# Performance work log

Measured on AMD Instinct MI355X. Metric: run time of the kernel, lower is better.

Reference implementation:

```python
import jax, jax.numpy as jnp
import numpy as np

N = 100_000      # nodes
E = 500_000      # bonds
DN = 128         # dim_node_embedding
DB = 64          # dim_bond_embedding
NTOK = 4         # num_bond_token
DIN = 2 * DN + 2 * DB  # 384
LEAKY = 0.001
LN_EPS = 1e-5
DIST_MAX = 20.0
STEP = 0.5


def _lrelu(v):
    return jnp.where(v >= 0, v, LEAKY * v)


def _layernorm(v, w, b):
    m = v.mean(-1, keepdims=True)
    var = ((v - m) ** 2).mean(-1, keepdims=True)
    return (v - m) / jnp.sqrt(var + LN_EPS) * w + b


def setup_inputs() -> dict:
    key = jax.random.key(0)
    ks = jax.random.split(key, 20)
    x = jax.random.normal(ks[0], (N, 3), dtype=jnp.float32) * 3.0
    pos = jax.random.normal(ks[1], (N, 3), dtype=jnp.float32)
    node_embedding = jax.random.normal(ks[2], (N, DN), dtype=jnp.float32)
    i0 = jax.random.randint(ks[3], (E,), 0, N)
    off = jax.random.randint(ks[4], (E,), 1, N)  # nonzero -> no self-bonds
    bond_index = jnp.stack([i0, (i0 + off) % N], axis=1).astype(jnp.int32)
    bond_types = jax.random.randint(ks[5], (E,), 0, NTOK).astype(jnp.int32)
    s = 0.02
    params = dict(
        bond_emb=jax.random.normal(ks[6], (NTOK, DB), dtype=jnp.float32),
        W0=jax.random.normal(ks[7], (DIN, DN), dtype=jnp.float32) * s,
        b0=jnp.zeros((DN,), jnp.float32),
        W1=jax.random.normal(ks[8], (DN, DN), dtype=jnp.float32) * s,
        b1=jnp.zeros((DN,), jnp.float32),
        ln1_w=jnp.ones((DN,), jnp.float32),
        ln1_b=jnp.zeros((DN,), jnp.float32),
        W2=jax.random.normal(ks[9], (DN, DN), dtype=jnp.float32) * s,
        b2=jnp.zeros((DN,), jnp.float32),
        ln2_w=jnp.ones((DN,), jnp.float32),
        ln2_b=jnp.zeros((DN,), jnp.float32),
        Wo=jax.random.normal(ks[10], (DN, 2), dtype=jnp.float32) * s,
        bo=jnp.zeros((2,), jnp.float32),
    )
    return dict(x=x, pos=pos, node_embedding=node_embedding,
                bond_index=bond_index, bond_types=bond_types, **params)


def reference(x, pos, node_embedding, bond_index, bond_types,
              bond_emb, W0, b0, W1, b1, ln1_w, ln1_b,
              W2, b2, ln2_w, ln2_b, Wo, bo):
    i = bond_index[:, 0]
    j = bond_index[:, 1]

    # ---- BondLength geometry ----
    diff = x[i] - x[j]                                   # [E,3]
    dist = jnp.linalg.norm(diff, axis=-1, keepdims=True)  # [E,1]
    u = diff / dist                                       # [E,3] unit j->i? (i-j)/d
    direction = jnp.stack([u, -u], axis=-1)               # [E,3,2]

    # ---- Smearing (gaussian RBF + overflow bin, normalized) ----
    offset = jnp.linspace(0.0, DIST_MAX, DB - 1, dtype=jnp.float32)  # [63]
    delta = DIST_MAX / (DB - 2)
    coeff = -0.5 / (delta * delta)
    rbf = jnp.exp(coeff * (dist - offset) ** 2)            # [E,63]
    ovf = (dist >= DIST_MAX).astype(x.dtype)               # [E,1]
    smear = jnp.concatenate([rbf, ovf], axis=-1)           # [E,64]
    smear = smear / smear.sum(axis=-1, keepdims=True)

    # ---- Edge MLP (LeakyMLP, num_layer=2, dim_end=2) ----
    feat = jnp.concatenate(
        [node_embedding[i], node_embedding[j], bond_emb[bond_types], smear],
        axis=-1)                                           # [E,384]
    h = _lrelu(feat @ W0 + b0)
    h = _lrelu(_layernorm(h @ W1 + b1, ln1_w, ln1_b))
    h = _lrelu(_layernorm(h @ W2 + b2, ln2_w, ln2_b))
    force = h @ Wo + bo                                    # [E,2]

    # ---- position update (scatter-add) ----
    update = force[:, None, :] * direction                 # [E,3,2]
    pos = pos.at[i].add(STEP * update[..., 0])
    pos = pos.at[j].add(STEP * update[..., 1])
    return pos
```

## Files before the change

### kernel.cpp

```cpp
#include <hip/hip_runtime.h>
#include <stdint.h>

#define N_EDGES 500000
#define N_NODES 100000
#define PREP_NG 2
#define TBINS 1280

typedef __attribute__((ext_vector_type(8))) short short8;
typedef __attribute__((ext_vector_type(4))) float floatx4;

__device__ __forceinline__ uint16_t f2bf(float f) {
  union { float f; uint32_t u; } cv; cv.f = f;
  uint32_t u = cv.u;
  return (uint16_t)((u + 0x7FFFu + ((u >> 16) & 1u)) >> 16);
}
__device__ __forceinline__ uint32_t pk2bf(float lo, float hi) {
  return __builtin_amdgcn_perm(__float_as_uint(hi), __float_as_uint(lo), 0x07060302u);
}
__device__ __forceinline__ uint16_t bftrunc(float f) {
  return (uint16_t)(__float_as_uint(f) >> 16);
}
__device__ __forceinline__ float bf2f_lo(uint32_t u) { return __uint_as_float(u << 16); }
__device__ __forceinline__ float bf2f_hi(uint32_t u) { return __uint_as_float(u & 0xFFFF0000u); }
__device__ __forceinline__ float lrelu(float v) { return fmaxf(v, 0.001f * v); }

__device__ __forceinline__ void gload_lds16(const uint16_t* g, uint16_t* l) {
  __builtin_amdgcn_global_load_lds(
      (const __attribute__((address_space(1))) void*)g,
      (__attribute__((address_space(3))) void*)l, 16, 0, 0);
}

__global__ void prep0_kernel(const float* __restrict__ W0, const float* __restrict__ b0,
                             const float* __restrict__ W1, const float* __restrict__ W2,
                             const float* __restrict__ bemb,
                             uint16_t* __restrict__ w0ab, uint16_t* __restrict__ w1f,
                             uint16_t* __restrict__ w2f, float* __restrict__ be0f,
                             const float* __restrict__ pos, float* __restrict__ out, int npos) {
  int id = blockIdx.x * 256 + threadIdx.x;
  if (id < 32768) {
    int f = id;
    int j = f & 7, lane = (f >> 3) & 63, ntt = (f >> 9) & 15, ks = f >> 13;
    int k = ks * 32 + (lane >> 4) * 8 + j;
    int row = (ntt < 8) ? k : (128 + k);
    int col = (ntt & 7) * 16 + (lane & 15);
    w0ab[f] = f2bf(W0[row * 128 + col]);
  } else if (id < 49152) {
    int f = id - 32768;
    int j = f & 7, lane = (f >> 3) & 63, nt = (f >> 9) & 7, ks = f >> 12;
    int k = ks * 32 + (lane >> 4) * 8 + j;
    w1f[f] = f2bf(W1[k * 128 + nt * 16 + (lane & 15)]);
  } else if (id < 65536) {
    int f = id - 49152;
    int j = f & 7, lane = (f >> 3) & 63, nt = (f >> 9) & 7, ks = f >> 12;
    int k = ks * 32 + (lane >> 4) * 8 + j;
    w2f[f] = f2bf(W2[k * 128 + nt * 16 + (lane & 15)]);
  } else if (id < 66048) {
    int t = id - 65536; int ty = t >> 7, n = t & 127;
    float s = b0[n];
    for (int kk = 0; kk < 64; ++kk) s += bemb[ty * 64 + kk] * W0[(256 + kk) * 128 + n];
    be0f[t] = s;
  } else if (id - 66048 < npos) {
    out[id - 66048] = pos[id - 66048];
  }
}

__global__ void prep_t_kernel(const float* __restrict__ W0, const float* __restrict__ be0f,
                              uint16_t* __restrict__ T) {
  __shared__ float rbf[64];
  int b = blockIdx.x;
  int t = threadIdx.x;
  float dist = (float)b * (1.0f / 32.0f);
  const float delta = 20.0f / 62.0f;
  const float coeff = -0.5f / (delta * delta);
  if (t < 64) {
    float v;
    if (t < 63) { float d = dist - (float)t * delta; v = __expf(coeff * d * d); }
    else v = (dist >= 20.0f) ? 1.0f : 0.0f;
    rbf[t] = v;
  }
  __syncthreads();
  float sum = 0.0f;
  for (int k = 0; k < 64; ++k) sum += rbf[k];
  float rs = 1.0f / sum;
  for (int o = t; o < 512; o += 256) {
    int ty = o >> 7, n = o & 127;
    float s = be0f[ty * 128 + n];
    for (int k = 0; k < 64; ++k) s += rbf[k] * rs * W0[(320 + k) * 128 + n];
    T[((size_t)(ty * TBINS + b)) * 128 + n] = f2bf(s);
  }
}

__global__ __attribute__((amdgpu_flat_work_group_size(256, 256), amdgpu_waves_per_eu(1, 4)))
void prep_p_kernel(const float* __restrict__ nemb, const uint16_t* __restrict__ w0ab,
                   uint16_t* __restrict__ Pa, uint16_t* __restrict__ Pb) {
  __shared__ __align__(16) uint16_t aLds[4 * PREP_NG * 16 * 136];
  const int tid = threadIdx.x;
  const int lane = tid & 63;
  const int wave = tid >> 6;
  const int n15 = lane & 15;
  const int quad = lane >> 4;
  uint16_t* myA = aLds + wave * (PREP_NG * 16 * 136);
  const int base = blockIdx.x * (64 * PREP_NG) + wave * (16 * PREP_NG);

  {
    const int le = lane >> 2, sub = lane & 3;
#pragma unroll
    for (int it = 0; it < PREP_NG; ++it) {
      int r = base + it * 16 + le; if (r >= N_NODES) r = N_NODES - 1;
      const float4* src = (const float4*)(nemb + (size_t)r * 128);
#pragma unroll
      for (int g = 0; g < 4; ++g) {
        float4 a = src[sub * 8 + g * 2], b = src[sub * 8 + g * 2 + 1];
        uint4 pk;
        pk.x = pk2bf(a.x, a.y); pk.y = pk2bf(a.z, a.w);
        pk.z = pk2bf(b.x, b.y); pk.w = pk2bf(b.z, b.w);
        *(uint4*)(myA + (it * 16 + le) * 136 + sub * 32 + g * 8) = pk;
      }
    }
  }

  const short8* wfv = (const short8*)w0ab + lane;
#pragma unroll
  for (int q = 0; q < 4; ++q) {
    short8 bfr[16];
#pragma unroll
    for (int ks = 0; ks < 4; ++ks)
#pragma unroll
      for (int nq = 0; nq < 4; ++nq)
        bfr[ks * 4 + nq] = wfv[(ks * 16 + q * 4 + nq) * 64];
#pragma unroll
    for (int it = 0; it < PREP_NG; ++it) {
      floatx4 acc[4];
#pragma unroll
      for (int nq = 0; nq < 4; ++nq) acc[nq] = (floatx4){0.f, 0.f, 0.f, 0.f};
#pragma unroll
      for (int ks = 0; ks < 4; ++ks) {
        short8 a = *(const short8*)(myA + (it * 16 + n15) * 136 + ks * 32 + quad * 8);
#pragma unroll
        for (int nq = 0; nq < 4; ++nq)
          acc[nq] = __builtin_amdgcn_mfma_f32_16x16x32_bf16(a, bfr[ks * 4 + nq], acc[nq], 0, 0, 0);
      }
      uint16_t* dst = (q < 2) ? Pa : Pb;
      int cbase = ((q & 1) * 4) * 16 + n15;
#pragma unroll
      for (int nq = 0; nq < 4; ++nq) {
        int c = cbase + nq * 16;
#pragma unroll
        for (int r = 0; r < 4; ++r) {
          int row = base + it * 16 + quad * 4 + r;
          if (row < N_NODES) dst[(size_t)row * 128 + c] = bftrunc(acc[nq][r]);
        }
      }
    }
  }
}

__device__ __forceinline__ void gemm_lds(const uint16_t* ws, const uint16_t* aRow,
                                         int lane, floatx4* acc) {
  short8 a[4];
#pragma unroll
  for (int ks = 0; ks < 4; ++ks) a[ks] = *(const short8*)(aRow + ks * 32);
#pragma unroll
  for (int ks = 0; ks < 4; ++ks)
#pragma unroll
    for (int nt = 0; nt < 8; ++nt) {
      short8 b = *(const short8*)(ws + (ks * 8 + nt) * 512 + lane * 8);
      acc[nt] = __builtin_amdgcn_mfma_f32_16x16x32_bf16(a[ks], b, acc[nt], 0, 0, 0);
    }
}

__global__ __attribute__((amdgpu_flat_work_group_size(256, 256)))
void bond_mlp_kernel(const float* __restrict__ x,
                     const int* __restrict__ bidx, const int* __restrict__ btyp,
                     const uint16_t* __restrict__ Pa, const uint16_t* __restrict__ Pb,
                     const uint16_t* __restrict__ Tt, const uint16_t* __restrict__ w1f,
                     const uint16_t* __restrict__ w2f,
                     const float* __restrict__ b1, const float* __restrict__ ln1w,
                     const float* __restrict__ ln1b,
                     const float* __restrict__ b2, const float* __restrict__ ln2w,
                     const float* __restrict__ ln2b,
                     const float* __restrict__ Wo, const float* __restrict__ bo,
                     float* __restrict__ out) {
  __shared__ __align__(16) uint16_t wstage[16384];
  __shared__ __align__(16) uint16_t hA_all[4 * 16 * 136];
  __shared__ float u_lds[64][3];
  __shared__ int ij_lds[64][2];

  const int tid = threadIdx.x;
  const int lane = tid & 63;
  const int wave = tid >> 6;
  const int n15 = lane & 15;
  const int quad = lane >> 4;

  uint16_t* hA = hA_all + wave * (16 * 136);

#pragma unroll
  for (int j = 0; j < 8; ++j)
    gload_lds16(w1f + (wave * 8 + j) * 512 + lane * 8, wstage + (wave * 8 + j) * 512);

  {
    const int le = lane >> 2, sub = lane & 3;
    const int gr = wave * 16 + le;
    const int ge = blockIdx.x * 64 + gr;
    const bool valid = ge < N_EDGES;
    int vi = 0, vj = 0, bt = 0;
    if (valid) { vi = bidx[2 * ge]; vj = bidx[2 * ge + 1]; bt = btyp[ge]; }
    float dx, dy, dz;
    if (valid) {
      dx = x[3 * vi]     - x[3 * vj];
      dy = x[3 * vi + 1] - x[3 * vj + 1];
      dz = x[3 * vi + 2] - x[3 * vj + 2];
    } else { dx = 1.0f; dy = 0.0f; dz = 0.0f; }
    float dist = sqrtf(dx * dx + dy * dy + dz * dz);
    float rinv = 1.0f / dist;
    if (sub == 0) {
      u_lds[gr][0] = dx * rinv; u_lds[gr][1] = dy * rinv; u_lds[gr][2] = dz * rinv;
      ij_lds[gr][0] = vi; ij_lds[gr][1] = vj;
    }
    float fb = fminf(dist, 39.5f) * 32.0f;
    int bi = (int)fb;
    float w = fb - (float)bi;
    const uint4* pa = (const uint4*)(Pa + (size_t)vi * 128 + sub * 32);
    const uint4* pb = (const uint4*)(Pb + (size_t)vj * 128 + sub * 32);
    const uint16_t* trow = Tt + ((size_t)(bt * TBINS + bi)) * 128 + sub * 32;
    const uint4* t0p = (const uint4*)trow;
    const uint4* t1p = (const uint4*)(trow + 128);
#pragma unroll
    for (int g = 0; g < 4; ++g) {
      uint4 av = pa[g], bv = pb[g], t0 = t0p[g], t1 = t1p[g];
      uint4 pk;
      {
        float lo = bf2f_lo(av.x) + bf2f_lo(bv.x), hi = bf2f_hi(av.x) + bf2f_hi(bv.x);
        float l0 = bf2f_lo(t0.x), l1 = bf2f_lo(t1.x), h0 = bf2f_hi(t0.x), h1 = bf2f_hi(t1.x);
        pk.x = pk2bf(lrelu(lo + l0 + w * (l1 - l0)), lrelu(hi + h0 + w * (h1 - h0)));
      }
      {
        float lo = bf2f_lo(av.y) + bf2f_lo(bv.y), hi = bf2f_hi(av.y) + bf2f_hi(bv.y);
        float l0 = bf2f_lo(t0.y), l1 = bf2f_lo(t1.y), h0 = bf2f_hi(t0.y), h1 = bf2f_hi(t1.y);
        pk.y = pk2bf(lrelu(lo + l0 + w * (l1 - l0)), lrelu(hi + h0 + w * (h1 - h0)));
      }
      {
        float lo = bf2f_lo(av.z) + bf2f_lo(bv.z), hi = bf2f_hi(av.z) + bf2f_hi(bv.z);
        float l0 = bf2f_lo(t0.z), l1 = bf2f_lo(t1.z), h0 = bf2f_hi(t0.z), h1 = bf2f_hi(t1.z);
        pk.z = pk2bf(lrelu(lo + l0 + w * (l1 - l0)), lrelu(hi + h0 + w * (h1 - h0)));
      }
      {
        float lo = bf2f_lo(av.w) + bf2f_lo(bv.w), hi = bf2f_hi(av.w) + bf2f_hi(bv.w);
        float l0 = bf2f_lo(t0.w), l1 = bf2f_lo(t1.w), h0 = bf2f_hi(t0.w), h1 = bf2f_hi(t1.w);
        pk.w = pk2bf(lrelu(lo + l0 + w * (l1 - l0)), lrelu(hi + h0 + w * (h1 - h0)));
      }
      *(uint4*)(hA + le * 136 + sub * 32 + g * 8) = pk;
    }
  }
  __syncthreads();

  const uint16_t* aRow = hA + n15 * 136 + quad * 8;

  floatx4 acc[8];
#pragma unroll
  for (int nt = 0; nt < 8; ++nt) acc[nt] = (floatx4){0.f, 0.f, 0.f, 0.f};
  gemm_lds(wstage, aRow, lane, acc);

  __syncthreads();
#pragma unroll
  for (int j = 0; j < 8; ++j)
    gload_lds16(w2f + (wave * 8 + j) * 512 + lane * 8, wstage + (wave * 8 + j) * 512);

  {
    float bv[8], wv[8], bb2[8];
#pragma unroll
    for (int nt = 0; nt < 8; ++nt) {
      int col = nt * 16 + n15;
      bv[nt] = b1[col]; wv[nt] = ln1w[col]; bb2[nt] = ln1b[col];
    }
    float s[4] = {0,0,0,0}, q[4] = {0,0,0,0};
#pragma unroll
    for (int nt = 0; nt < 8; ++nt)
#pragma unroll
      for (int r = 0; r < 4; ++r) { float v = acc[nt][r] + bv[nt]; s[r] += v; q[r] += v * v; }
#pragma unroll
    for (int m = 1; m <= 8; m <<= 1)
#pragma unroll
      for (int r = 0; r < 4; ++r) { s[r] += __shfl_xor(s[r], m); q[r] += __shfl_xor(q[r], m); }
    float mean[4], rstd[4];
#pragma unroll
    for (int r = 0; r < 4; ++r) {
      mean[r] = s[r] * (1.0f / 128.0f);
      float var = q[r] * (1.0f / 128.0f) - mean[r] * mean[r];
      rstd[r] = rsqrtf(var + 1e-5f);
    }
#pragma unroll
    for (int nt = 0; nt < 8; ++nt)
#pragma unroll
      for (int r = 0; r < 4; ++r) {
        float v = acc[nt][r] + bv[nt];
        float vn = (v - mean[r]) * rstd[r] * wv[nt] + bb2[nt];
        hA[(quad * 4 + r) * 136 + nt * 16 + n15] = bftrunc(lrelu(vn));
      }
  }
  __syncthreads();

#pragma unroll
  for (int nt = 0; nt < 8; ++nt) acc[nt] = (floatx4){0.f, 0.f, 0.f, 0.f};
  gemm_lds(wstage, aRow, lane, acc);

  {
    float bv[8], wv[8], bb2[8], wo0[8], wo1[8];
#pragma unroll
    for (int nt = 0; nt < 8; ++nt) {
      int col = nt * 16 + n15;
      bv[nt] = b2[col]; wv[nt] = ln2w[col]; bb2[nt] = ln2b[col];
      wo0[nt] = Wo[2 * col]; wo1[nt] = Wo[2 * col + 1];
    }
    float s[4] = {0,0,0,0}, q[4] = {0,0,0,0};
#pragma unroll
    for (int nt = 0; nt < 8; ++nt)
#pragma unroll
      for (int r = 0; r < 4; ++r) { float v = acc[nt][r] + bv[nt]; s[r] += v; q[r] += v * v; }
#pragma unroll
    for (int m = 1; m <= 8; m <<= 1)
#pragma unroll
      for (int r = 0; r < 4; ++r) { s[r] += __shfl_xor(s[r], m); q[r] += __shfl_xor(q[r], m); }
    float mean[4], rstd[4];
#pragma unroll
    for (int r = 0; r < 4; ++r) {
      mean[r] = s[r] * (1.0f / 128.0f);
      float var = q[r] * (1.0f / 128.0f) - mean[r] * mean[r];
      rstd[r] = rsqrtf(var + 1e-5f);
    }
    float f0[4] = {0,0,0,0}, f1[4] = {0,0,0,0};
#pragma unroll
    for (int nt = 0; nt < 8; ++nt)
#pragma unroll
      for (int r = 0; r < 4; ++r) {
        float v = acc[nt][r] + bv[nt];
        float vn = lrelu((v - mean[r]) * rstd[r] * wv[nt] + bb2[nt]);
        f0[r] += vn * wo0[nt];
        f1[r] += vn * wo1[nt];
      }
#pragma unroll
    for (int m = 1; m <= 8; m <<= 1)
#pragma unroll
      for (int r = 0; r < 4; ++r) { f0[r] += __shfl_xor(f0[r], m); f1[r] += __shfl_xor(f1[r], m); }

    if (n15 < 4) {
      int gr = wave * 16 + quad * 4 + n15;
      int ge2 = blockIdx.x * 64 + gr;
      if (ge2 < N_EDGES) {
        float F0 = (n15 == 0) ? f0[0] : (n15 == 1) ? f0[1] : (n15 == 2) ? f0[2] : f0[3];
        float F1 = (n15 == 0) ? f1[0] : (n15 == 1) ? f1[1] : (n15 == 2) ? f1[2] : f1[3];
        F0 += bo[0]; F1 += bo[1];
        float ux = u_lds[gr][0], uy = u_lds[gr][1], uz = u_lds[gr][2];
        int ii = ij_lds[gr][0], jj = ij_lds[gr][1];
        float c0 = 0.5f * F0;
        float c1 = -0.5f * F1;
        atomicAdd(out + 3 * ii,     c0 * ux);
        atomicAdd(out + 3 * ii + 1, c0 * uy);
        atomicAdd(out + 3 * ii + 2, c0 * uz);
        atomicAdd(out + 3 * jj,     c1 * ux);
        atomicAdd(out + 3 * jj + 1, c1 * uy);
        atomicAdd(out + 3 * jj + 2, c1 * uz);
      }
    }
  }
}

extern "C" void kernel_launch(void* const* d_in, const int* in_sizes, int n_in,
                              void* d_out, int out_size, void* d_ws, size_t ws_size,
                              hipStream_t stream) {
  const float* x    = (const float*)d_in[0];
  const float* pos  = (const float*)d_in[1];
  const float* nemb = (const float*)d_in[2];
  const int*   bidx = (const int*)d_in[3];
  const int*   btyp = (const int*)d_in[4];
  const float* bemb = (const float*)d_in[5];
  const float* W0   = (const float*)d_in[6];
  const float* b0   = (const float*)d_in[7];
  const float* W1   = (const float*)d_in[8];
  const float* b1   = (const float*)d_in[9];
  const float* ln1w = (const float*)d_in[10];
  const float* ln1b = (const float*)d_in[11];
  const float* W2   = (const float*)d_in[12];
  const float* b2   = (const float*)d_in[13];
  const float* ln2w = (const float*)d_in[14];
  const float* ln2b = (const float*)d_in[15];
  const float* Wo   = (const float*)d_in[16];
  const float* bo   = (const float*)d_in[17];
  float* out = (float*)d_out;

  uint16_t* w0ab = (uint16_t*)d_ws;
  uint16_t* w1f  = w0ab + 32768;
  uint16_t* w2f  = w1f + 16384;
  float*    be0f = (float*)(w2f + 16384);
  uint16_t* Tt   = (uint16_t*)(be0f + 512);
  uint16_t* Pa   = Tt + (size_t)4 * TBINS * 128;
  uint16_t* Pb   = Pa + (size_t)N_NODES * 128;

  prep0_kernel<<<(66048 + out_size + 255) / 256, 256, 0, stream>>>(
      W0, b0, W1, W2, bemb, w0ab, w1f, w2f, be0f, pos, out, out_size);
  prep_t_kernel<<<TBINS, 256, 0, stream>>>(W0, be0f, Tt);
  prep_p_kernel<<<(N_NODES + 64 * PREP_NG - 1) / (64 * PREP_NG), 256, 0, stream>>>(
      nemb, w0ab, Pa, Pb);
  bond_mlp_kernel<<<(N_EDGES + 63) / 64, 256, 0, stream>>>(
      x, bidx, btyp, Pa, Pb, Tt, w1f, w2f,
      b1, ln1w, ln1b, b2, ln2w, ln2b, Wo, bo, out);
}
```

Measured before the change: 352.0 us.

## Read MLP weights from global in bond kernel and merge prep launches

```diff
diff --git a/kernel.cpp b/kernel.cpp
--- a/kernel.cpp
+++ b/kernel.cpp
@@ -23,12 +23,6 @@
 __device__ __forceinline__ float bf2f_lo(uint32_t u) { return __uint_as_float(u << 16); }
 __device__ __forceinline__ float bf2f_hi(uint32_t u) { return __uint_as_float(u & 0xFFFF0000u); }
 __device__ __forceinline__ float lrelu(float v) { return fmaxf(v, 0.001f * v); }
-
-__device__ __forceinline__ void gload_lds16(const uint16_t* g, uint16_t* l) {
-  __builtin_amdgcn_global_load_lds(
-      (const __attribute__((address_space(1))) void*)g,
-      (__attribute__((address_space(3))) void*)l, 16, 0, 0);
-}
 
 __global__ void prep0_kernel(const float* __restrict__ W0, const float* __restrict__ b0,
                              const float* __restrict__ W1, const float* __restrict__ W2,
@@ -64,43 +58,46 @@
   }
 }
 
-__global__ void prep_t_kernel(const float* __restrict__ W0, const float* __restrict__ be0f,
-                              uint16_t* __restrict__ T) {
+__global__ __attribute__((amdgpu_flat_work_group_size(256, 256)))
+void prep_tp_kernel(const float* __restrict__ W0, const float* __restrict__ be0f,
+                    uint16_t* __restrict__ T,
+                    const float* __restrict__ nemb, const uint16_t* __restrict__ w0ab,
+                    uint16_t* __restrict__ Pa, uint16_t* __restrict__ Pb) {
+  __shared__ __align__(16) uint16_t aLds[4 * PREP_NG * 16 * 136];
   __shared__ float rbf[64];
-  int b = blockIdx.x;
-  int t = threadIdx.x;
-  float dist = (float)b * (1.0f / 32.0f);
-  const float delta = 20.0f / 62.0f;
-  const float coeff = -0.5f / (delta * delta);
-  if (t < 64) {
-    float v;
-    if (t < 63) { float d = dist - (float)t * delta; v = __expf(coeff * d * d); }
-    else v = (dist >= 20.0f) ? 1.0f : 0.0f;
-    rbf[t] = v;
-  }
-  __syncthreads();
-  float sum = 0.0f;
-  for (int k = 0; k < 64; ++k) sum += rbf[k];
-  float rs = 1.0f / sum;
-  for (int o = t; o < 512; o += 256) {
-    int ty = o >> 7, n = o & 127;
-    float s = be0f[ty * 128 + n];
-    for (int k = 0; k < 64; ++k) s += rbf[k] * rs * W0[(320 + k) * 128 + n];
-    T[((size_t)(ty * TBINS + b)) * 128 + n] = f2bf(s);
-  }
-}
-
-__global__ __attribute__((amdgpu_flat_work_group_size(256, 256), amdgpu_waves_per_eu(1, 4)))
-void prep_p_kernel(const float* __restrict__ nemb, const uint16_t* __restrict__ w0ab,
-                   uint16_t* __restrict__ Pa, uint16_t* __restrict__ Pb) {
-  __shared__ __align__(16) uint16_t aLds[4 * PREP_NG * 16 * 136];
   const int tid = threadIdx.x;
+
+  if (blockIdx.x < TBINS) {
+    int b = blockIdx.x;
+    float dist = (float)b * (1.0f / 32.0f);
+    const float delta = 20.0f / 62.0f;
+    const float coeff = -0.5f / (delta * delta);
+    if (tid < 64) {
+      float v;
+      if (tid < 63) { float d = dist - (float)tid * delta; v = __expf(coeff * d * d); }
+      else v = (dist >= 20.0f) ? 1.0f : 0.0f;
+      rbf[tid] = v;
+    }
+    __syncthreads();
+    float sum = 0.0f;
+    for (int k = 0; k < 64; ++k) sum += rbf[k];
+    float rs = 1.0f / sum;
+    for (int o = tid; o < 512; o += 256) {
+      int ty = o >> 7, n = o & 127;
+      float s = be0f[ty * 128 + n];
+      for (int k = 0; k < 64; ++k) s += rbf[k] * rs * W0[(320 + k) * 128 + n];
+      T[((size_t)(ty * TBINS + b)) * 128 + n] = f2bf(s);
+    }
+    return;
+  }
+
+  const int pblk = blockIdx.x - TBINS;
   const int lane = tid & 63;
   const int wave = tid >> 6;
   const int n15 = lane & 15;
   const int quad = lane >> 4;
   uint16_t* myA = aLds + wave * (PREP_NG * 16 * 136);
-  const int base = blockIdx.x * (64 * PREP_NG) + wave * (16 * PREP_NG);
+  const int base = pblk * (64 * PREP_NG) + wave * (16 * PREP_NG);
 
   {
     const int le = lane >> 2, sub = lane & 3;
@@ -155,21 +152,20 @@
   }
 }
 
-__device__ __forceinline__ void gemm_lds(const uint16_t* ws, const uint16_t* aRow,
-                                         int lane, floatx4* acc) {
+__device__ __forceinline__ void gemm_g(const uint16_t* __restrict__ wf, const uint16_t* aRow,
+                                       int lane, floatx4* acc) {
   short8 a[4];
 #pragma unroll
   for (int ks = 0; ks < 4; ++ks) a[ks] = *(const short8*)(aRow + ks * 32);
+  const short8* wv = (const short8*)wf + lane;
 #pragma unroll
   for (int ks = 0; ks < 4; ++ks)
 #pragma unroll
-    for (int nt = 0; nt < 8; ++nt) {
-      short8 b = *(const short8*)(ws + (ks * 8 + nt) * 512 + lane * 8);
-      acc[nt] = __builtin_amdgcn_mfma_f32_16x16x32_bf16(a[ks], b, acc[nt], 0, 0, 0);
-    }
-}
-
-__global__ __attribute__((amdgpu_flat_work_group_size(256, 256)))
+    for (int nt = 0; nt < 8; ++nt)
+      acc[nt] = __builtin_amdgcn_mfma_f32_16x16x32_bf16(a[ks], wv[(ks * 8 + nt) * 64], acc[nt], 0, 0, 0);
+}
+
+__global__ __attribute__((amdgpu_flat_work_group_size(256, 256), amdgpu_waves_per_eu(4)))
 void bond_mlp_kernel(const float* __restrict__ x,
                      const int* __restrict__ bidx, const int* __restrict__ btyp,
                      const uint16_t* __restrict__ Pa, const uint16_t* __restrict__ Pb,
@@ -181,7 +177,6 @@
                      const float* __restrict__ ln2b,
                      const float* __restrict__ Wo, const float* __restrict__ bo,
                      float* __restrict__ out) {
-  __shared__ __align__(16) uint16_t wstage[16384];
   __shared__ __align__(16) uint16_t hA_all[4 * 16 * 136];
   __shared__ float u_lds[64][3];
   __shared__ int ij_lds[64][2];
@@ -193,10 +188,6 @@
   const int quad = lane >> 4;
 
   uint16_t* hA = hA_all + wave * (16 * 136);
-
-#pragma unroll
-  for (int j = 0; j < 8; ++j)
-    gload_lds16(w1f + (wave * 8 + j) * 512 + lane * 8, wstage + (wave * 8 + j) * 512);
 
   {
     const int le = lane >> 2, sub = lane & 3;
@@ -252,19 +243,13 @@
       *(uint4*)(hA + le * 136 + sub * 32 + g * 8) = pk;
     }
   }
-  __syncthreads();
 
   const uint16_t* aRow = hA + n15 * 136 + quad * 8;
 
   floatx4 acc[8];
 #pragma unroll
   for (int nt = 0; nt < 8; ++nt) acc[nt] = (floatx4){0.f, 0.f, 0.f, 0.f};
-  gemm_lds(wstage, aRow, lane, acc);
-
-  __syncthreads();
-#pragma unroll
-  for (int j = 0; j < 8; ++j)
-    gload_lds16(w2f + (wave * 8 + j) * 512 + lane * 8, wstage + (wave * 8 + j) * 512);
+  gemm_g(w1f, aRow, lane, acc);
 
   {
     float bv[8], wv[8], bb2[8];
@@ -298,11 +283,10 @@
         hA[(quad * 4 + r) * 136 + nt * 16 + n15] = bftrunc(lrelu(vn));
       }
   }
-  __syncthreads();
 
 #pragma unroll
   for (int nt = 0; nt < 8; ++nt) acc[nt] = (floatx4){0.f, 0.f, 0.f, 0.f};
-  gemm_lds(wstage, aRow, lane, acc);
+  gemm_g(w2f, aRow, lane, acc);
 
   {
     float bv[8], wv[8], bb2[8], wo0[8], wo1[8];
@@ -396,11 +380,12 @@
   uint16_t* Pa   = Tt + (size_t)4 * TBINS * 128;
   uint16_t* Pb   = Pa + (size_t)N_NODES * 128;
 
+  const int nblkP = (N_NODES + 64 * PREP_NG - 1) / (64 * PREP_NG);
+
   prep0_kernel<<<(66048 + out_size + 255) / 256, 256, 0, stream>>>(
       W0, b0, W1, W2, bemb, w0ab, w1f, w2f, be0f, pos, out, out_size);
-  prep_t_kernel<<<TBINS, 256, 0, stream>>>(W0, be0f, Tt);
-  prep_p_kernel<<<(N_NODES + 64 * PREP_NG - 1) / (64 * PREP_NG), 256, 0, stream>>>(
-      nemb, w0ab, Pa, Pb);
+  prep_tp_kernel<<<TBINS + nblkP, 256, 0, stream>>>(
+      W0, be0f, Tt, nemb, w0ab, Pa, Pb);
   bond_mlp_kernel<<<(N_EDGES + 63) / 64, 256, 0, stream>>>(
       x, bidx, btyp, Pa, Pb, Tt, w1f, w2f,
       b1, ln1w, ln1b, b2, ln2w, ln2b, Wo, bo, out);
```

New measurement: 339.6 us. 1.04x faster.
